# Optimization experiments

Measured on AMD Instinct MI355X. Metric: run time of the kernel, lower is better.

## Reference

```python
import jax, jax.numpy as jnp
import numpy as np


def gcn_conv(x, W, b, src, dst, num_nodes):
    # h = X W  (tiny GEMM)
    h = x @ W
    # symmetric degree normalization with self-loops: D^-1/2 (A+I) D^-1/2
    deg = jax.ops.segment_sum(jnp.ones_like(dst, dtype=h.dtype), dst, num_segments=num_nodes)
    dinv = jnp.where(deg > 0, jax.lax.rsqrt(jnp.maximum(deg, 1e-12)), 0.0)
    norm = dinv[src] * dinv[dst]                      # [E]
    msg = h[src] * norm[:, None]                      # gather + scale, [E, F]
    out = jax.ops.segment_sum(msg, dst, num_segments=num_nodes)  # scatter-add, [N, F]
    return out + b


def reference(x, edge_index, W1, b1, W2, b2):
    num_nodes = x.shape[0]
    # add self-loops once (PyG GCNConv adds them inside each conv; identical edges both layers)
    loop = jnp.arange(num_nodes, dtype=edge_index.dtype)
    src = jnp.concatenate([edge_index[0], loop])
    dst = jnp.concatenate([edge_index[1], loop])
    h = gcn_conv(x, W1, b1, src, dst, num_nodes)
    h = jax.nn.relu(h)
    out = gcn_conv(h, W2, b2, src, dst, num_nodes)
    return out


def setup_inputs() -> dict:
    key = jax.random.key(0)
    k1, k2, k3, k4 = jax.random.split(key, 4)
    N, E, C_in, C_hid, C_out = 100000, 3200000, 128, 16, 128
    x = jax.random.normal(k1, (N, C_in), dtype=jnp.float32)
    edge_index = jax.random.randint(k2, (2, E), 0, N, dtype=jnp.int64)
    W1 = jax.random.normal(k3, (C_in, C_hid), dtype=jnp.float32) * (1.0 / np.sqrt(C_in))
    b1 = jnp.zeros((C_hid,), dtype=jnp.float32)
    W2 = jax.random.normal(k4, (C_hid, C_out), dtype=jnp.float32) * (1.0 / np.sqrt(C_hid))
    b2 = jnp.zeros((C_out,), dtype=jnp.float32)
    return {"x": x, "edge_index": edge_index, "W1": W1, "b1": b1, "W2": W2, "b2": b2}
```

## Files before the change

kernel.cpp:

```cpp
#include <hip/hip_runtime.h>
#include <hip/hip_fp16.h>

typedef _Float16 half8 __attribute__((ext_vector_type(8)));
typedef _Float16 half4 __attribute__((ext_vector_type(4)));
typedef float f32x4 __attribute__((ext_vector_type(4)));
typedef unsigned uint4v __attribute__((ext_vector_type(4)));

#define RANGE    512
#define RSH      9
#define CAP      17408
#define T_TILE   4096

__global__ void init_gcursor(int* __restrict__ gcursor, int NB) {
    int t = blockIdx.x * blockDim.x + threadIdx.x;
    if (t < NB) gcursor[t] = t * CAP;
}


__global__ __launch_bounds__(256) void binpass_gemm1(const int* __restrict__ src,
                                                     const int* __restrict__ dst, int E,
                                                     int* __restrict__ gcursor,
                                                     unsigned* __restrict__ pairbuf,
                                                     int binBlocks,
                                                     const float* __restrict__ x,
                                                     const float* __restrict__ W1,
                                                     __half* __restrict__ g1, int N) {
    if (blockIdx.x >= binBlocks) {
        int wave = threadIdx.x >> 6;
        int lane = threadIdx.x & 63;
        int R0 = (blockIdx.x - binBlocks) * 64 + wave * 16;
        if (R0 >= N) return;
        int m = lane & 15;
        int kb = (lane >> 4) * 8;
        int row = R0 + m;
        int rowc = min(row, N - 1);

        half8 bfrag[4];
#pragma unroll
        for (int kk = 0; kk < 4; ++kk) {
#pragma unroll
            for (int j = 0; j < 8; ++j)
                bfrag[kk][j] = (_Float16)W1[(kk * 32 + kb + j) * 16 + m];
        }
        const float* xr = x + (size_t)rowc * 128;
        float4 u[8];
#pragma unroll
        for (int kk = 0; kk < 4; ++kk) {
            u[2 * kk]     = *reinterpret_cast<const float4*>(xr + kk * 32 + kb);
            u[2 * kk + 1] = *reinterpret_cast<const float4*>(xr + kk * 32 + kb + 4);
        }
        f32x4 acc = {0.f, 0.f, 0.f, 0.f};
#pragma unroll
        for (int kk = 0; kk < 4; ++kk) {
            half8 a;
            a[0] = (_Float16)u[2 * kk].x;     a[1] = (_Float16)u[2 * kk].y;
            a[2] = (_Float16)u[2 * kk].z;     a[3] = (_Float16)u[2 * kk].w;
            a[4] = (_Float16)u[2 * kk + 1].x; a[5] = (_Float16)u[2 * kk + 1].y;
            a[6] = (_Float16)u[2 * kk + 1].z; a[7] = (_Float16)u[2 * kk + 1].w;
            acc = __builtin_amdgcn_mfma_f32_16x16x32_f16(a, bfrag[kk], acc, 0, 0, 0);
        }
#pragma unroll
        for (int i = 0; i < 4; ++i) {
            int r = R0 + (lane >> 4) * 4 + i;
            if (r < N) g1[(size_t)r * 16 + m] = __float2half(acc[i]);
        }
        return;
    }
    __shared__ unsigned sbuf[T_TILE];
    __shared__ unsigned char sbk[T_TILE];
    __shared__ int lcount[256], loff[256], lplace[256], gbase[256];
    int t = threadIdx.x;
    int base = blockIdx.x * T_TILE;
    int ecount = min(T_TILE, E - base);

    lcount[t] = 0;
    __syncthreads();

    unsigned pk[16];
    int bn[16];
#pragma unroll
    for (int k4 = 0; k4 < 4; ++k4) {
        int i = base + (t + k4 * 256) * 4;
        if (i + 3 < E) {
            int4 sv = *reinterpret_cast<const int4*>(src + i);
            int4 dv = *reinterpret_cast<const int4*>(dst + i);
            int ss[4] = {sv.x, sv.y, sv.z, sv.w};
            int dd[4] = {dv.x, dv.y, dv.z, dv.w};
#pragma unroll
            for (int m = 0; m < 4; ++m) {
                int k = k4 * 4 + m;
                bn[k] = dd[m] >> RSH;
                pk[k] = ((unsigned)ss[m] << RSH) | (unsigned)(dd[m] & (RANGE - 1));
                atomicAdd(&lcount[bn[k]], 1);
            }
        } else {
#pragma unroll
            for (int m = 0; m < 4; ++m) {
                int k = k4 * 4 + m;
                int ii = i + m;
                if (ii < E) {
                    int s = src[ii], d = dst[ii];
                    bn[k] = d >> RSH;
                    pk[k] = ((unsigned)s << RSH) | (unsigned)(d & (RANGE - 1));
                    atomicAdd(&lcount[bn[k]], 1);
                } else bn[k] = -1;
            }
        }
    }
    __syncthreads();
    loff[t] = lcount[t];
    __syncthreads();
    for (int off = 1; off < 256; off <<= 1) {
        int u = (t >= off) ? loff[t - off] : 0;
        __syncthreads();
        loff[t] += u;
        __syncthreads();
    }
    int ex = loff[t] - lcount[t];
    __syncthreads();
    loff[t] = ex;
    lplace[t] = ex;
    if (lcount[t] > 0) gbase[t] = atomicAdd(&gcursor[t], lcount[t]);
    __syncthreads();
#pragma unroll
    for (int k = 0; k < 16; ++k) {
        if (bn[k] >= 0) {
            int pos = atomicAdd(&lplace[bn[k]], 1);
            sbuf[pos] = pk[k];
            sbk[pos] = (unsigned char)bn[k];
        }
    }
    __syncthreads();
    for (int i = t; i < ecount; i += 256) {
        int b = sbk[i];
        pairbuf[gbase[b] + (i - loff[b])] = sbuf[i];
    }
}

__global__ __launch_bounds__(256) void bucketscan(const int* __restrict__ gcursor, int NB,
                                                  int* __restrict__ bbase,
                                                  int* __restrict__ rowptr, int N) {
    __shared__ int sd[256];
    int t = threadIdx.x;
    int c = (t < NB) ? (gcursor[t] - t * CAP) : 0;
    sd[t] = c;
    __syncthreads();
    for (int off = 1; off < 256; off <<= 1) {
        int u = (t >= off) ? sd[t - off] : 0;
        __syncthreads();
        sd[t] += u;
        __syncthreads();
    }
    if (t < NB) bbase[t] = sd[t] - c;
    if (t == 255) { bbase[NB] = sd[255]; rowptr[N] = sd[255]; }
}

__global__ __launch_bounds__(512) void bucket_build(const unsigned* __restrict__ pairbuf,
                                                    const int* __restrict__ gcursor,
                                                    const int* __restrict__ bbase, int N,
                                                    int* __restrict__ rowptr,
                                                    float* __restrict__ dinv,
                                                    int* __restrict__ eidx) {
    __shared__ int lcnt[RANGE];
    __shared__ int lsc[RANGE];
    int b = blockIdx.x, t = threadIdx.x;
    int cnt = gcursor[b] - b * CAP;
    const unsigned* pb = pairbuf + (size_t)b * CAP;

    lcnt[t] = 0;
    __syncthreads();
    for (int i = t; i < cnt; i += 512) atomicAdd(&lcnt[pb[i] & (RANGE - 1)], 1);
    __syncthreads();
    lsc[t] = lcnt[t];
    __syncthreads();
    for (int off = 1; off < 512; off <<= 1) {
        int u = (t >= off) ? lsc[t - off] : 0;
        __syncthreads();
        lsc[t] += u;
        __syncthreads();
    }
    int ex = lsc[t] - lcnt[t];
    int gb = bbase[b];
    int node = b * RANGE + t;
    if (node < N) {
        rowptr[node] = gb + ex;
        dinv[node] = rsqrtf((float)lcnt[t] + 1.0f);
    }
    __syncthreads();
    lsc[t] = gb + ex;
    __syncthreads();
    for (int i = t; i < cnt; i += 512) {
        unsigned p = pb[i];
        int pos = atomicAdd(&lsc[p & (RANGE - 1)], 1);
        eidx[pos] = (int)(p >> RSH);
    }
}


__device__ __forceinline__ void unp8(uint4v v, float* f) {
#pragma unroll
    for (int k = 0; k < 4; ++k) {
        unsigned w = v[k];
        __half2 h2 = *reinterpret_cast<__half2*>(&w);
        float2 t = __half22float2(h2);
        f[2 * k] = t.x; f[2 * k + 1] = t.y;
    }
}

__device__ __forceinline__ void acc8(float* a, uint4v v) {
#pragma unroll
    for (int k = 0; k < 4; ++k) {
        unsigned w = v[k];
        __half2 h2 = *reinterpret_cast<__half2*>(&w);
        float2 t = __half22float2(h2);
        a[2 * k]     += t.x;
        a[2 * k + 1] += t.y;
    }
}

__device__ __forceinline__ uint4v pk8(const float* o) {
    uint4v r;
#pragma unroll
    for (int k = 0; k < 4; ++k) {
        __half2 h2 = __floats2half2_rn(o[2 * k], o[2 * k + 1]);
        r[k] = *reinterpret_cast<unsigned*>(&h2);
    }
    return r;
}


__global__ __launch_bounds__(256) void scale_g1(__half* __restrict__ g1,
                                                const float* __restrict__ dinv, int N) {
    int gid = blockIdx.x * blockDim.x + threadIdx.x;
    if (gid >= N * 2) return;
    int node = gid >> 1, f0 = (gid & 1) * 8;
    float di = dinv[node];
    uint4v v = *reinterpret_cast<const uint4v*>(g1 + node * 16 + f0);
    float f[8];
    unp8(v, f);
#pragma unroll
    for (int k = 0; k < 8; ++k) f[k] *= di;
    *reinterpret_cast<uint4v*>(g1 + node * 16 + f0) = pk8(f);
}


__global__ __launch_bounds__(256) void gather1_kernel(const int* __restrict__ rowptr,
                                                      const int* __restrict__ eidx,
                                                      const __half* __restrict__ g1,
                                                      const float* __restrict__ dinv,
                                                      const float* __restrict__ b1,
                                                      __half* __restrict__ g2, int N) {
    int gid = blockIdx.x * blockDim.x + threadIdx.x;
    int d = gid >> 3;
    if (d >= N) return;
    int sub = threadIdx.x & 7;
    int h = sub & 1, es = sub >> 1;
    int f0 = h * 8;
    int lo = rowptr[d], hi = rowptr[d + 1];
    float di = dinv[d];
    uint4v svh = *reinterpret_cast<const uint4v*>(g1 + d * 16 + f0);

    float a[8] = {0, 0, 0, 0, 0, 0, 0, 0};
    int j = lo + es;
    for (; j + 28 < hi; j += 32) {
        int s[8];
#pragma unroll
        for (int k = 0; k < 8; ++k) s[k] = eidx[j + 4 * k];
        uint4v v[8];
#pragma unroll
        for (int k = 0; k < 8; ++k)
            v[k] = *reinterpret_cast<const uint4v*>(g1 + s[k] * 16 + f0);
#pragma unroll
        for (int k = 0; k < 8; ++k) acc8(a, v[k]);
    }
    for (; j < hi; j += 4) {
        int s = eidx[j];
        uint4v v = *reinterpret_cast<const uint4v*>(g1 + s * 16 + f0);
        acc8(a, v);
    }
#pragma unroll
    for (int k = 0; k < 8; ++k) {
        a[k] += __shfl_xor(a[k], 2);
        a[k] += __shfl_xor(a[k], 4);
    }
    if (es == 0) {
        float sf[8];
        unp8(svh, sf);
        f32x4 bb0 = *reinterpret_cast<const f32x4*>(b1 + f0);
        f32x4 bb1 = *reinterpret_cast<const f32x4*>(b1 + f0 + 4);
        float o[8];
#pragma unroll
        for (int k = 0; k < 4; ++k) {
            o[k]     = fmaxf(di * (a[k] + sf[k]) + bb0[k], 0.0f) * di;
            o[k + 4] = fmaxf(di * (a[k + 4] + sf[k + 4]) + bb1[k], 0.0f) * di;
        }
        *reinterpret_cast<uint4v*>(g2 + d * 16 + f0) = pk8(o);
    }
}


__global__ __launch_bounds__(256) void gather2_gemm2(const int* __restrict__ rowptr,
                                                     const int* __restrict__ eidx,
                                                     const __half* __restrict__ g2,
                                                     const float* __restrict__ dinv,
                                                     const float* __restrict__ W2,
                                                     const float* __restrict__ b2,
                                                     float* __restrict__ out, int N) {
    int gid = blockIdx.x * blockDim.x + threadIdx.x;
    int wid = gid >> 6;
    int lane = threadIdx.x & 63;
    int base = wid * 16;
    if (base >= N) return;
    int nl = lane & 15;
    int q = lane >> 4;
    int es = q & 1;
    int h = lane >> 5;
    int f0 = h * 8;
    int d = base + nl;
    int dc = min(d, N - 1);
    int lo = rowptr[dc], hi = rowptr[dc + 1];

    float a[8] = {0, 0, 0, 0, 0, 0, 0, 0};
    int j = lo + es;
    for (; j + 14 < hi; j += 16) {
        int s[8];
#pragma unroll
        for (int k = 0; k < 8; ++k) s[k] = eidx[j + 2 * k];
        uint4v v[8];
#pragma unroll
        for (int k = 0; k < 8; ++k)
            v[k] = *reinterpret_cast<const uint4v*>(g2 + s[k] * 16 + f0);
#pragma unroll
        for (int k = 0; k < 8; ++k) acc8(a, v[k]);
    }
    for (; j < hi; j += 2) {
        int s = eidx[j];
        uint4v v = *reinterpret_cast<const uint4v*>(g2 + s * 16 + f0);
        acc8(a, v);
    }
#pragma unroll
    for (int k = 0; k < 8; ++k) a[k] += __shfl_xor(a[k], 16);

    float di = dinv[dc];
    uint4v sv = *reinterpret_cast<const uint4v*>(g2 + dc * 16 + f0);
    float sf[8];
    unp8(sv, sf);
    float af[8];
#pragma unroll
    for (int k = 0; k < 8; ++k) af[k] = di * (a[k] + sf[k]);

    int hi4 = es * 4;
    half4 afrag;
#pragma unroll
    for (int jj = 0; jj < 4; ++jj) afrag[jj] = (_Float16)af[hi4 + jj];

    f32x4 dacc[8];
#pragma unroll
    for (int ct = 0; ct < 8; ++ct) {
        half4 bfrag;
#pragma unroll
        for (int jj = 0; jj < 4; ++jj)
            bfrag[jj] = (_Float16)W2[(q * 4 + jj) * 128 + ct * 16 + nl];
        f32x4 z = {0.f, 0.f, 0.f, 0.f};
        dacc[ct] = __builtin_amdgcn_mfma_f32_16x16x16f16(afrag, bfrag, z, 0, 0, 0);
    }

    float bias[8];
#pragma unroll
    for (int ct = 0; ct < 8; ++ct) bias[ct] = b2[ct * 16 + nl];

    int rbase = base + q * 4;
#pragma unroll
    for (int i = 0; i < 4; ++i) {
        int r = rbase + i;
        if (r < N) {
            float* orow = out + (size_t)r * 128 + nl;
#pragma unroll
            for (int ct = 0; ct < 8; ++ct) orow[ct * 16] = dacc[ct][i] + bias[ct];
        }
    }
}


extern "C" void kernel_launch(void* const* d_in, const int* in_sizes, int n_in,
                              void* d_out, int out_size, void* d_ws, size_t ws_size,
                              hipStream_t stream) {
    const float* x  = (const float*)d_in[0];
    const int*   ei = (const int*)d_in[1];
    const float* W1 = (const float*)d_in[2];
    const float* b1 = (const float*)d_in[3];
    const float* W2 = (const float*)d_in[4];
    const float* b2 = (const float*)d_in[5];
    float* out = (float*)d_out;

    const int N = in_sizes[0] / 128;
    const int E = in_sizes[1] / 2;
    const int* src = ei;
    const int* dst = ei + E;
    const int NB = (N + RANGE - 1) / RANGE;

    unsigned* pairbuf = (unsigned*)d_ws;
    int* gcursor = (int*)(pairbuf + (size_t)NB * CAP);
    int* bbase   = gcursor + NB;
    int* rowptr  = bbase + (NB + 1);
    int* eidx    = rowptr + (N + 1);
    float* dinv  = (float*)(eidx + E);
    __half* g1 = (__half*)(dinv + N);
    __half* g2 = g1 + 16 * N;

    const int B = 256;
    const int binBlocks  = (E + T_TILE - 1) / T_TILE;
    const int gemmBlocks = (N + 63) / 64;
    init_gcursor<<<1, B, 0, stream>>>(gcursor, NB);
    binpass_gemm1<<<binBlocks + gemmBlocks, B, 0, stream>>>(src, dst, E, gcursor, pairbuf,
                                                            binBlocks, x, W1, g1, N);
    bucketscan<<<1, B, 0, stream>>>(gcursor, NB, bbase, rowptr, N);
    bucket_build<<<NB, 512, 0, stream>>>(pairbuf, gcursor, bbase, N, rowptr, dinv, eidx);
    scale_g1<<<(N * 2 + B - 1) / B, B, 0, stream>>>(g1, dinv, N);
    gather1_kernel<<<(N * 8 + B - 1) / B, B, 0, stream>>>(rowptr, eidx, g1, dinv, b1, g2, N);
    gather2_gemm2<<<(N * 4 + B - 1) / B, B, 0, stream>>>(rowptr, eidx, g2, dinv, W2, b2, out, N);
}
```

Measured before the change: 140.1 us.

## Fuse g1 degree scaling into bucket build; restructure gather2 to 128-thread groups

The separate scale_g1 kernel is removed, and the dinv scaling of g1 now happens inside bucket_build right after each node's degree is known, saving one launch and one read/write pass over g1. gather2_gemm2 now uses two waves per 16-node group: 4 edge streams per node across each wave, and each wave handles one 8-feature half. The reduced sums are exchanged through shared memory so each wave computes half of the output columns with MFMA. The change doubles the gather parallelism per node and halves the per-wave MFMA and store work, at the cost of a block-wide sync and shared-memory traffic.

```diff
diff --git a/kernel.cpp b/kernel.cpp
--- a/kernel.cpp
+++ b/kernel.cpp
@@ -14,6 +14,38 @@
 __global__ void init_gcursor(int* __restrict__ gcursor, int NB) {
     int t = blockIdx.x * blockDim.x + threadIdx.x;
     if (t < NB) gcursor[t] = t * CAP;
+}
+
+
+__device__ __forceinline__ void unp8(uint4v v, float* f) {
+#pragma unroll
+    for (int k = 0; k < 4; ++k) {
+        unsigned w = v[k];
+        __half2 h2 = *reinterpret_cast<__half2*>(&w);
+        float2 t = __half22float2(h2);
+        f[2 * k] = t.x; f[2 * k + 1] = t.y;
+    }
+}
+
+__device__ __forceinline__ void acc8(float* a, uint4v v) {
+#pragma unroll
+    for (int k = 0; k < 4; ++k) {
+        unsigned w = v[k];
+        __half2 h2 = *reinterpret_cast<__half2*>(&w);
+        float2 t = __half22float2(h2);
+        a[2 * k]     += t.x;
+        a[2 * k + 1] += t.y;
+    }
+}
+
+__device__ __forceinline__ uint4v pk8(const float* o) {
+    uint4v r;
+#pragma unroll
+    for (int k = 0; k < 4; ++k) {
+        __half2 h2 = __floats2half2_rn(o[2 * k], o[2 * k + 1]);
+        r[k] = *reinterpret_cast<unsigned*>(&h2);
+    }
+    return r;
 }
 
 
@@ -160,7 +192,8 @@
                                                     const int* __restrict__ bbase, int N,
                                                     int* __restrict__ rowptr,
                                                     float* __restrict__ dinv,
-                                                    int* __restrict__ eidx) {
+                                                    int* __restrict__ eidx,
+                                                    __half* __restrict__ g1) {
     __shared__ int lcnt[RANGE];
     __shared__ int lsc[RANGE];
     int b = blockIdx.x, t = threadIdx.x;
@@ -184,7 +217,20 @@
     int node = b * RANGE + t;
     if (node < N) {
         rowptr[node] = gb + ex;
-        dinv[node] = rsqrtf((float)lcnt[t] + 1.0f);
+        float di = rsqrtf((float)lcnt[t] + 1.0f);
+        dinv[node] = di;
+        __half* gr = g1 + (size_t)node * 16;
+        uint4v v0 = *reinterpret_cast<const uint4v*>(gr);
+        uint4v v1 = *reinterpret_cast<const uint4v*>(gr + 8);
+        float f[8];
+        unp8(v0, f);
+#pragma unroll
+        for (int k = 0; k < 8; ++k) f[k] *= di;
+        *reinterpret_cast<uint4v*>(gr) = pk8(f);
+        unp8(v1, f);
+#pragma unroll
+        for (int k = 0; k < 8; ++k) f[k] *= di;
+        *reinterpret_cast<uint4v*>(gr + 8) = pk8(f);
     }
     __syncthreads();
     lsc[t] = gb + ex;
@@ -194,53 +240,6 @@
         int pos = atomicAdd(&lsc[p & (RANGE - 1)], 1);
         eidx[pos] = (int)(p >> RSH);
     }
-}
-
-
-__device__ __forceinline__ void unp8(uint4v v, float* f) {
-#pragma unroll
-    for (int k = 0; k < 4; ++k) {
-        unsigned w = v[k];
-        __half2 h2 = *reinterpret_cast<__half2*>(&w);
-        float2 t = __half22float2(h2);
-        f[2 * k] = t.x; f[2 * k + 1] = t.y;
-    }
-}
-
-__device__ __forceinline__ void acc8(float* a, uint4v v) {
-#pragma unroll
-    for (int k = 0; k < 4; ++k) {
-        unsigned w = v[k];
-        __half2 h2 = *reinterpret_cast<__half2*>(&w);
-        float2 t = __half22float2(h2);
-        a[2 * k]     += t.x;
-        a[2 * k + 1] += t.y;
-    }
-}
-
-__device__ __forceinline__ uint4v pk8(const float* o) {
-    uint4v r;
-#pragma unroll
-    for (int k = 0; k < 4; ++k) {
-        __half2 h2 = __floats2half2_rn(o[2 * k], o[2 * k + 1]);
-        r[k] = *reinterpret_cast<unsigned*>(&h2);
-    }
-    return r;
-}
-
-
-__global__ __launch_bounds__(256) void scale_g1(__half* __restrict__ g1,
-                                                const float* __restrict__ dinv, int N) {
-    int gid = blockIdx.x * blockDim.x + threadIdx.x;
-    if (gid >= N * 2) return;
-    int node = gid >> 1, f0 = (gid & 1) * 8;
-    float di = dinv[node];
-    uint4v v = *reinterpret_cast<const uint4v*>(g1 + node * 16 + f0);
-    float f[8];
-    unp8(v, f);
-#pragma unroll
-    for (int k = 0; k < 8; ++k) f[k] *= di;
-    *reinterpret_cast<uint4v*>(g1 + node * 16 + f0) = pk8(f);
 }
 
 
@@ -258,7 +257,7 @@
     int f0 = h * 8;
     int lo = rowptr[d], hi = rowptr[d + 1];
     float di = dinv[d];
-    uint4v svh = *reinterpret_cast<const uint4v*>(g1 + d * 16 + f0);
+    uint4v svh = *reinterpret_cast<const uint4v*>(g1 + (size_t)d * 16 + f0);
 
     float a[8] = {0, 0, 0, 0, 0, 0, 0, 0};
     int j = lo + es;
@@ -269,13 +268,13 @@
         uint4v v[8];
 #pragma unroll
         for (int k = 0; k < 8; ++k)
-            v[k] = *reinterpret_cast<const uint4v*>(g1 + s[k] * 16 + f0);
+            v[k] = *reinterpret_cast<const uint4v*>(g1 + (size_t)s[k] * 16 + f0);
 #pragma unroll
         for (int k = 0; k < 8; ++k) acc8(a, v[k]);
     }
     for (; j < hi; j += 4) {
         int s = eidx[j];
-        uint4v v = *reinterpret_cast<const uint4v*>(g1 + s * 16 + f0);
+        uint4v v = *reinterpret_cast<const uint4v*>(g1 + (size_t)s * 16 + f0);
         acc8(a, v);
     }
 #pragma unroll
@@ -294,7 +293,7 @@
             o[k]     = fmaxf(di * (a[k] + sf[k]) + bb0[k], 0.0f) * di;
             o[k + 4] = fmaxf(di * (a[k + 4] + sf[k + 4]) + bb1[k], 0.0f) * di;
         }
-        *reinterpret_cast<uint4v*>(g2 + d * 16 + f0) = pk8(o);
+        *reinterpret_cast<uint4v*>(g2 + (size_t)d * 16 + f0) = pk8(o);
     }
 }
 
@@ -306,77 +305,83 @@
                                                      const float* __restrict__ W2,
                                                      const float* __restrict__ b2,
                                                      float* __restrict__ out, int N) {
-    int gid = blockIdx.x * blockDim.x + threadIdx.x;
-    int wid = gid >> 6;
+    __shared__ float sm[2][16][17];
+    int grp = threadIdx.x >> 7;
+    int G = blockIdx.x * 2 + grp;
+    int base = G * 16;
+    int w = (threadIdx.x >> 6) & 1;
     int lane = threadIdx.x & 63;
-    int base = wid * 16;
-    if (base >= N) return;
     int nl = lane & 15;
-    int q = lane >> 4;
-    int es = q & 1;
-    int h = lane >> 5;
-    int f0 = h * 8;
+    int es = lane >> 4;
+    int q = es;
+    int f0 = w * 8;
     int d = base + nl;
     int dc = min(d, N - 1);
     int lo = rowptr[dc], hi = rowptr[dc + 1];
+    float di = dinv[dc];
+    uint4v sv = *reinterpret_cast<const uint4v*>(g2 + (size_t)dc * 16 + f0);
 
     float a[8] = {0, 0, 0, 0, 0, 0, 0, 0};
     int j = lo + es;
-    for (; j + 14 < hi; j += 16) {
+    for (; j + 28 < hi; j += 32) {
         int s[8];
 #pragma unroll
-        for (int k = 0; k < 8; ++k) s[k] = eidx[j + 2 * k];
+        for (int k = 0; k < 8; ++k) s[k] = eidx[j + 4 * k];
         uint4v v[8];
 #pragma unroll
         for (int k = 0; k < 8; ++k)
-            v[k] = *reinterpret_cast<const uint4v*>(g2 + s[k] * 16 + f0);
+            v[k] = *reinterpret_cast<const uint4v*>(g2 + (size_t)s[k] * 16 + f0);
 #pragma unroll
         for (int k = 0; k < 8; ++k) acc8(a, v[k]);
     }
-    for (; j < hi; j += 2) {
+    for (; j < hi; j += 4) {
         int s = eidx[j];
-        uint4v v = *reinterpret_cast<const uint4v*>(g2 + s * 16 + f0);
+        uint4v v = *reinterpret_cast<const uint4v*>(g2 + (size_t)s * 16 + f0);
         acc8(a, v);
     }
 #pragma unroll
-    for (int k = 0; k < 8; ++k) a[k] += __shfl_xor(a[k], 16);
-
-    float di = dinv[dc];
-    uint4v sv = *reinterpret_cast<const uint4v*>(g2 + dc * 16 + f0);
+    for (int k = 0; k < 8; ++k) {
+        a[k] += __shfl_xor(a[k], 16);
+        a[k] += __shfl_xor(a[k], 32);
+    }
+
     float sf[8];
     unp8(sv, sf);
-    float af[8];
-#pragma unroll
-    for (int k = 0; k < 8; ++k) af[k] = di * (a[k] + sf[k]);
-
-    int hi4 = es * 4;
+    if (lane < 16) {
+#pragma unroll
+        for (int k = 0; k < 8; ++k) sm[grp][nl][f0 + k] = di * (a[k] + sf[k]);
+    }
+    __syncthreads();
+
     half4 afrag;
 #pragma unroll
-    for (int jj = 0; jj < 4; ++jj) afrag[jj] = (_Float16)af[hi4 + jj];
-
-    f32x4 dacc[8];
-#pragma unroll
-    for (int ct = 0; ct < 8; ++ct) {
+    for (int jj = 0; jj < 4; ++jj) afrag[jj] = (_Float16)sm[grp][nl][q * 4 + jj];
+
+    f32x4 dacc[4];
+#pragma unroll
+    for (int c = 0; c < 4; ++c) {
+        int ct = w * 4 + c;
         half4 bfrag;
 #pragma unroll
         for (int jj = 0; jj < 4; ++jj)
             bfrag[jj] = (_Float16)W2[(q * 4 + jj) * 128 + ct * 16 + nl];
         f32x4 z = {0.f, 0.f, 0.f, 0.f};
-        dacc[ct] = __builtin_amdgcn_mfma_f32_16x16x16f16(afrag, bfrag, z, 0, 0, 0);
-    }
-
-    float bias[8];
-#pragma unroll
-    for (int ct = 0; ct < 8; ++ct) bias[ct] = b2[ct * 16 + nl];
-
-    int rbase = base + q * 4;
-#pragma unroll
-    for (int i = 0; i < 4; ++i) {
-        int r = rbase + i;
-        if (r < N) {
-            float* orow = out + (size_t)r * 128 + nl;
-#pragma unroll
-            for (int ct = 0; ct < 8; ++ct) orow[ct * 16] = dacc[ct][i] + bias[ct];
+        dacc[c] = __builtin_amdgcn_mfma_f32_16x16x16f16(afrag, bfrag, z, 0, 0, 0);
+    }
+
+    if (base < N) {
+        float bias[4];
+#pragma unroll
+        for (int c = 0; c < 4; ++c) bias[c] = b2[(w * 4 + c) * 16 + nl];
+        int rbase = base + q * 4;
+#pragma unroll
+        for (int i = 0; i < 4; ++i) {
+            int r = rbase + i;
+            if (r < N) {
+                float* orow = out + (size_t)r * 128 + nl;
+#pragma unroll
+                for (int c = 0; c < 4; ++c) orow[(w * 4 + c) * 16] = dacc[c][i] + bias[c];
+            }
         }
     }
 }
@@ -415,8 +420,8 @@
     binpass_gemm1<<<binBlocks + gemmBlocks, B, 0, stream>>>(src, dst, E, gcursor, pairbuf,
                                                             binBlocks, x, W1, g1, N);
     bucketscan<<<1, B, 0, stream>>>(gcursor, NB, bbase, rowptr, N);
-    bucket_build<<<NB, 512, 0, stream>>>(pairbuf, gcursor, bbase, N, rowptr, dinv, eidx);
-    scale_g1<<<(N * 2 + B - 1) / B, B, 0, stream>>>(g1, dinv, N);
+    bucket_build<<<NB, 512, 0, stream>>>(pairbuf, gcursor, bbase, N, rowptr, dinv, eidx, g1);
     gather1_kernel<<<(N * 8 + B - 1) / B, B, 0, stream>>>(rowptr, eidx, g1, dinv, b1, g2, N);
-    gather2_gemm2<<<(N * 4 + B - 1) / B, B, 0, stream>>>(rowptr, eidx, g2, dinv, W2, b2, out, N);
-}
+    const int grpBlocks = ((N + 15) / 16 + 1) / 2;
+    gather2_gemm2<<<grpBlocks, B, 0, stream>>>(rowptr, eidx, g2, dinv, W2, b2, out, N);
+}
```

Result: slower. 148.3 us (+5.9%).

## Fold bucket scan and g1 scaling into bucket_build, cache pairs in LDS

Applied to the files above, without the earlier changes.

Removes the single-block bucketscan and scale_g1 kernels. Each bucket_build block now redoes the prefix scan over bucket counts itself and scales its g1 rows by dinv inline. It also stages its bucket's pairs in shared memory so the second pass reads LDS instead of global memory. The aim is to cut two launches and one global pass over pairbuf. In exchange, every block repeats a small scan and uses about 70KB of LDS, which limits occupancy.

```diff
diff --git a/kernel.cpp b/kernel.cpp
--- a/kernel.cpp
+++ b/kernel.cpp
@@ -14,6 +14,38 @@
 __global__ void init_gcursor(int* __restrict__ gcursor, int NB) {
     int t = blockIdx.x * blockDim.x + threadIdx.x;
     if (t < NB) gcursor[t] = t * CAP;
+}
+
+
+__device__ __forceinline__ void unp8(uint4v v, float* f) {
+#pragma unroll
+    for (int k = 0; k < 4; ++k) {
+        unsigned w = v[k];
+        __half2 h2 = *reinterpret_cast<__half2*>(&w);
+        float2 t = __half22float2(h2);
+        f[2 * k] = t.x; f[2 * k + 1] = t.y;
+    }
+}
+
+__device__ __forceinline__ void acc8(float* a, uint4v v) {
+#pragma unroll
+    for (int k = 0; k < 4; ++k) {
+        unsigned w = v[k];
+        __half2 h2 = *reinterpret_cast<__half2*>(&w);
+        float2 t = __half22float2(h2);
+        a[2 * k]     += t.x;
+        a[2 * k + 1] += t.y;
+    }
+}
+
+__device__ __forceinline__ uint4v pk8(const float* o) {
+    uint4v r;
+#pragma unroll
+    for (int k = 0; k < 4; ++k) {
+        __half2 h2 = __floats2half2_rn(o[2 * k], o[2 * k + 1]);
+        r[k] = *reinterpret_cast<unsigned*>(&h2);
+    }
+    return r;
 }
 
 
@@ -137,39 +169,38 @@
     }
 }
 
-__global__ __launch_bounds__(256) void bucketscan(const int* __restrict__ gcursor, int NB,
-                                                  int* __restrict__ bbase,
-                                                  int* __restrict__ rowptr, int N) {
-    __shared__ int sd[256];
-    int t = threadIdx.x;
-    int c = (t < NB) ? (gcursor[t] - t * CAP) : 0;
-    sd[t] = c;
-    __syncthreads();
-    for (int off = 1; off < 256; off <<= 1) {
-        int u = (t >= off) ? sd[t - off] : 0;
-        __syncthreads();
-        sd[t] += u;
-        __syncthreads();
-    }
-    if (t < NB) bbase[t] = sd[t] - c;
-    if (t == 255) { bbase[NB] = sd[255]; rowptr[N] = sd[255]; }
-}
 
 __global__ __launch_bounds__(512) void bucket_build(const unsigned* __restrict__ pairbuf,
                                                     const int* __restrict__ gcursor,
-                                                    const int* __restrict__ bbase, int N,
+                                                    int NB, int N, int E,
                                                     int* __restrict__ rowptr,
                                                     float* __restrict__ dinv,
-                                                    int* __restrict__ eidx) {
+                                                    int* __restrict__ eidx,
+                                                    __half* __restrict__ g1) {
+    __shared__ unsigned spair[CAP];
     __shared__ int lcnt[RANGE];
     __shared__ int lsc[RANGE];
+    __shared__ int sscan[256];
     int b = blockIdx.x, t = threadIdx.x;
+
+    if (t < 256) sscan[t] = (t < NB) ? (gcursor[t] - t * CAP) : 0;
+    if (t < RANGE) lcnt[t] = 0;
+    __syncthreads();
+    for (int off = 1; off < 256; off <<= 1) {
+        int u = (t >= off && t < 256) ? sscan[t - off] : 0;
+        __syncthreads();
+        if (t < 256) sscan[t] += u;
+        __syncthreads();
+    }
+    int gb = (b == 0) ? 0 : sscan[b - 1];
     int cnt = gcursor[b] - b * CAP;
     const unsigned* pb = pairbuf + (size_t)b * CAP;
 
-    lcnt[t] = 0;
-    __syncthreads();
-    for (int i = t; i < cnt; i += 512) atomicAdd(&lcnt[pb[i] & (RANGE - 1)], 1);
+    for (int i = t; i < cnt; i += 512) {
+        unsigned p = pb[i];
+        spair[i] = p;
+        atomicAdd(&lcnt[p & (RANGE - 1)], 1);
+    }
     __syncthreads();
     lsc[t] = lcnt[t];
     __syncthreads();
@@ -180,67 +211,33 @@
         __syncthreads();
     }
     int ex = lsc[t] - lcnt[t];
-    int gb = bbase[b];
     int node = b * RANGE + t;
     if (node < N) {
         rowptr[node] = gb + ex;
-        dinv[node] = rsqrtf((float)lcnt[t] + 1.0f);
-    }
+        float di = rsqrtf((float)lcnt[t] + 1.0f);
+        dinv[node] = di;
+        __half* gr = g1 + (size_t)node * 16;
+        uint4v v0 = *reinterpret_cast<const uint4v*>(gr);
+        uint4v v1 = *reinterpret_cast<const uint4v*>(gr + 8);
+        float f[8];
+        unp8(v0, f);
+#pragma unroll
+        for (int k = 0; k < 8; ++k) f[k] *= di;
+        *reinterpret_cast<uint4v*>(gr) = pk8(f);
+        unp8(v1, f);
+#pragma unroll
+        for (int k = 0; k < 8; ++k) f[k] *= di;
+        *reinterpret_cast<uint4v*>(gr + 8) = pk8(f);
+    }
+    if (b == 0 && t == 0) rowptr[N] = E;
     __syncthreads();
     lsc[t] = gb + ex;
     __syncthreads();
     for (int i = t; i < cnt; i += 512) {
-        unsigned p = pb[i];
+        unsigned p = spair[i];
         int pos = atomicAdd(&lsc[p & (RANGE - 1)], 1);
         eidx[pos] = (int)(p >> RSH);
     }
-}
-
-
-__device__ __forceinline__ void unp8(uint4v v, float* f) {
-#pragma unroll
-    for (int k = 0; k < 4; ++k) {
-        unsigned w = v[k];
-        __half2 h2 = *reinterpret_cast<__half2*>(&w);
-        float2 t = __half22float2(h2);
-        f[2 * k] = t.x; f[2 * k + 1] = t.y;
-    }
-}
-
-__device__ __forceinline__ void acc8(float* a, uint4v v) {
-#pragma unroll
-    for (int k = 0; k < 4; ++k) {
-        unsigned w = v[k];
-        __half2 h2 = *reinterpret_cast<__half2*>(&w);
-        float2 t = __half22float2(h2);
-        a[2 * k]     += t.x;
-        a[2 * k + 1] += t.y;
-    }
-}
-
-__device__ __forceinline__ uint4v pk8(const float* o) {
-    uint4v r;
-#pragma unroll
-    for (int k = 0; k < 4; ++k) {
-        __half2 h2 = __floats2half2_rn(o[2 * k], o[2 * k + 1]);
-        r[k] = *reinterpret_cast<unsigned*>(&h2);
-    }
-    return r;
-}
-
-
-__global__ __launch_bounds__(256) void scale_g1(__half* __restrict__ g1,
-                                                const float* __restrict__ dinv, int N) {
-    int gid = blockIdx.x * blockDim.x + threadIdx.x;
-    if (gid >= N * 2) return;
-    int node = gid >> 1, f0 = (gid & 1) * 8;
-    float di = dinv[node];
-    uint4v v = *reinterpret_cast<const uint4v*>(g1 + node * 16 + f0);
-    float f[8];
-    unp8(v, f);
-#pragma unroll
-    for (int k = 0; k < 8; ++k) f[k] *= di;
-    *reinterpret_cast<uint4v*>(g1 + node * 16 + f0) = pk8(f);
 }
 
 
@@ -258,7 +255,7 @@
     int f0 = h * 8;
     int lo = rowptr[d], hi = rowptr[d + 1];
     float di = dinv[d];
-    uint4v svh = *reinterpret_cast<const uint4v*>(g1 + d * 16 + f0);
+    uint4v svh = *reinterpret_cast<const uint4v*>(g1 + (size_t)d * 16 + f0);
 
     float a[8] = {0, 0, 0, 0, 0, 0, 0, 0};
     int j = lo + es;
@@ -269,13 +266,13 @@
         uint4v v[8];
 #pragma unroll
         for (int k = 0; k < 8; ++k)
-            v[k] = *reinterpret_cast<const uint4v*>(g1 + s[k] * 16 + f0);
+            v[k] = *reinterpret_cast<const uint4v*>(g1 + (size_t)s[k] * 16 + f0);
 #pragma unroll
         for (int k = 0; k < 8; ++k) acc8(a, v[k]);
     }
     for (; j < hi; j += 4) {
         int s = eidx[j];
-        uint4v v = *reinterpret_cast<const uint4v*>(g1 + s * 16 + f0);
+        uint4v v = *reinterpret_cast<const uint4v*>(g1 + (size_t)s * 16 + f0);
         acc8(a, v);
     }
 #pragma unroll
@@ -294,7 +291,7 @@
             o[k]     = fmaxf(di * (a[k] + sf[k]) + bb0[k], 0.0f) * di;
             o[k + 4] = fmaxf(di * (a[k + 4] + sf[k + 4]) + bb1[k], 0.0f) * di;
         }
-        *reinterpret_cast<uint4v*>(g2 + d * 16 + f0) = pk8(o);
+        *reinterpret_cast<uint4v*>(g2 + (size_t)d * 16 + f0) = pk8(o);
     }
 }
 
@@ -329,20 +326,20 @@
         uint4v v[8];
 #pragma unroll
         for (int k = 0; k < 8; ++k)
-            v[k] = *reinterpret_cast<const uint4v*>(g2 + s[k] * 16 + f0);
+            v[k] = *reinterpret_cast<const uint4v*>(g2 + (size_t)s[k] * 16 + f0);
 #pragma unroll
         for (int k = 0; k < 8; ++k) acc8(a, v[k]);
     }
     for (; j < hi; j += 2) {
         int s = eidx[j];
-        uint4v v = *reinterpret_cast<const uint4v*>(g2 + s * 16 + f0);
+        uint4v v = *reinterpret_cast<const uint4v*>(g2 + (size_t)s * 16 + f0);
         acc8(a, v);
     }
 #pragma unroll
     for (int k = 0; k < 8; ++k) a[k] += __shfl_xor(a[k], 16);
 
     float di = dinv[dc];
-    uint4v sv = *reinterpret_cast<const uint4v*>(g2 + dc * 16 + f0);
+    uint4v sv = *reinterpret_cast<const uint4v*>(g2 + (size_t)dc * 16 + f0);
     float sf[8];
     unp8(sv, sf);
     float af[8];
@@ -401,8 +398,7 @@
 
     unsigned* pairbuf = (unsigned*)d_ws;
     int* gcursor = (int*)(pairbuf + (size_t)NB * CAP);
-    int* bbase   = gcursor + NB;
-    int* rowptr  = bbase + (NB + 1);
+    int* rowptr  = gcursor + NB;
     int* eidx    = rowptr + (N + 1);
     float* dinv  = (float*)(eidx + E);
     __half* g1 = (__half*)(dinv + N);
@@ -414,9 +410,7 @@
     init_gcursor<<<1, B, 0, stream>>>(gcursor, NB);
     binpass_gemm1<<<binBlocks + gemmBlocks, B, 0, stream>>>(src, dst, E, gcursor, pairbuf,
                                                             binBlocks, x, W1, g1, N);
-    bucketscan<<<1, B, 0, stream>>>(gcursor, NB, bbase, rowptr, N);
-    bucket_build<<<NB, 512, 0, stream>>>(pairbuf, gcursor, bbase, N, rowptr, dinv, eidx);
-    scale_g1<<<(N * 2 + B - 1) / B, B, 0, stream>>>(g1, dinv, N);
+    bucket_build<<<NB, 512, 0, stream>>>(pairbuf, gcursor, NB, N, E, rowptr, dinv, eidx, g1);
     gather1_kernel<<<(N * 8 + B - 1) / B, B, 0, stream>>>(rowptr, eidx, g1, dinv, b1, g2, N);
     gather2_gemm2<<<(N * 4 + B - 1) / B, B, 0, stream>>>(rowptr, eidx, g2, dinv, W2, b2, out, N);
 }
```

After: 136.7 us. 2.4% less time.
